# Kernel tuning notes

Measured on AMD Instinct MI355X. Metric: run time of the kernel, lower is better.

## Reference

```python
import jax, jax.numpy as jnp
import numpy as np

N, T, H, D = 384, 384, 768, 128  # turns, per-turn seq len, hidden, qk proj dim


def setup_inputs() -> dict:
    key = jax.random.key(0)
    kx, kwq, kwk, kbq, kbk = jax.random.split(key, 5)
    x = jax.random.normal(kx, (N, T, H), dtype=jnp.float32)
    Wq = jax.random.normal(kwq, (H, D), dtype=jnp.float32) / np.sqrt(H).astype(np.float32)
    bq = jax.random.normal(kbq, (D,), dtype=jnp.float32) * 0.02
    Wk = jax.random.normal(kwk, (H, D), dtype=jnp.float32) / np.sqrt(H).astype(np.float32)
    bk = jax.random.normal(kbk, (D,), dtype=jnp.float32) * 0.02
    return {"x": x, "Wq": Wq, "bq": bq, "Wk": Wk, "bk": bk}


def reference(x, Wq, bq, Wk, bk):
    # x: [N, T, H] -> q, k: [N, T, D]
    q = x @ Wq + bq
    k = x @ Wk + bk
    # Per-position dot products across turns: s[i, j, t] = <q[i,t], k[j,t]> / sqrt(D)
    s = jnp.einsum('itd,jtd->ijt', q, k) / jnp.sqrt(jnp.asarray(D, x.dtype))
    # Causal over turns: row i attends to turns j <= i. The original does a
    # JOINT softmax over all (j, t) pairs in rows 0..i (flattened), per i.
    causal = jnp.arange(N)[:, None] >= jnp.arange(N)[None, :]  # [N, N]
    s = jnp.where(causal[:, :, None], s, -jnp.inf)
    alpha = jax.nn.softmax(s.reshape(N, N * T), axis=-1).reshape(N, N, T)
    # new_x[i, t, :] = sum_j alpha[i, j, t] * x[j, t, :]
    out = jnp.einsum('ijt,jth->ith', alpha, x)
    # Row 0 is a pass-through in the original (the i == 0 branch).
    out = out.at[0].set(x[0])
    return out
```

## Files before the change

### kernel.cpp

```cpp
#include <hip/hip_runtime.h>
#include <hip/hip_bf16.h>
#include <math.h>

#define NT 384
#define TL 384
#define HD 768
#define DD 128
#define PT_T 86016

typedef __attribute__((ext_vector_type(8))) short bf16x8;
typedef __attribute__((ext_vector_type(8))) unsigned short u16x8;
typedef __attribute__((ext_vector_type(4))) float f32x4;

__device__ __forceinline__ unsigned short f2b(float f) {
    union { float f; unsigned int u; } v; v.f = f;
    unsigned int r = v.u + 0x7FFFu + ((v.u >> 16) & 1u);
    return (unsigned short)(r >> 16);
}

__global__ __launch_bounds__(256) void kw_prep(
    const float* __restrict__ Wq, const float* __restrict__ Wk,
    unsigned short* __restrict__ Wt)
{
    const int idx = blockIdx.x * 256 + threadIdx.x;
    const int k = idx >> 8, n = idx & 255;
    const float v = (n < DD) ? Wq[(size_t)k * DD + n] : Wk[(size_t)k * DD + (n - DD)];
    Wt[(size_t)n * HD + k] = f2b(v);
}

__global__ __launch_bounds__(256, 3) void k_proj(
    const float* __restrict__ x, const unsigned short* __restrict__ Wt,
    const float* __restrict__ bq, const float* __restrict__ bk,
    unsigned short* __restrict__ qg, unsigned short* __restrict__ kg)
{
    __shared__ unsigned short As[64 * 64];
    __shared__ unsigned short os2[64 * 264];
    const int tid = threadIdx.x;
    const int lane = tid & 63;
    const int w = tid >> 6;
    const int row0 = blockIdx.x * 64;
    const int n0w = w * 64;
    const int lr = lane & 15;
    const int lg = lane >> 4;

    f32x4 acc[4][4];
    #pragma unroll
    for (int m = 0; m < 4; ++m)
        #pragma unroll
        for (int n = 0; n < 4; ++n) acc[m][n] = (f32x4){0.f, 0.f, 0.f, 0.f};

    const int sm = tid >> 2;
    const int sc0 = (tid & 3) * 2;

    for (int k0 = 0; k0 < HD; k0 += 64) {
        __syncthreads();
        {
            const float* xp = x + (size_t)(row0 + sm) * HD + k0 + (tid & 3) * 16;
            u16x8 v0, v1;
            #pragma unroll
            for (int u4 = 0; u4 < 2; ++u4) {
                float4 f = *(const float4*)(xp + u4 * 4);
                v0[u4*4+0] = f2b(f.x); v0[u4*4+1] = f2b(f.y);
                v0[u4*4+2] = f2b(f.z); v0[u4*4+3] = f2b(f.w);
            }
            #pragma unroll
            for (int u4 = 0; u4 < 2; ++u4) {
                float4 f = *(const float4*)(xp + 8 + u4 * 4);
                v1[u4*4+0] = f2b(f.x); v1[u4*4+1] = f2b(f.y);
                v1[u4*4+2] = f2b(f.z); v1[u4*4+3] = f2b(f.w);
            }
            *(u16x8*)&As[sm * 64 + ((sc0     ^ (sm & 7)) * 8)] = v0;
            *(u16x8*)&As[sm * 64 + (((sc0+1) ^ (sm & 7)) * 8)] = v1;
        }
        __syncthreads();
        #pragma unroll
        for (int kk = 0; kk < 2; ++kk) {
            bf16x8 a[4], b[4];
            #pragma unroll
            for (int m = 0; m < 4; ++m) {
                const int mi = m * 16 + lr;
                const int phys = (lg + kk * 4) ^ (mi & 7);
                a[m] = *(const bf16x8*)&As[mi * 64 + phys * 8];
            }
            #pragma unroll
            for (int n = 0; n < 4; ++n) {
                const int ncol = n0w + n * 16 + lr;
                b[n] = *(const bf16x8*)(Wt + (size_t)ncol * HD + k0 + kk * 32 + lg * 8);
            }
            #pragma unroll
            for (int m = 0; m < 4; ++m)
                #pragma unroll
                for (int n = 0; n < 4; ++n)
                    acc[m][n] = __builtin_amdgcn_mfma_f32_16x16x32_bf16(a[m], b[n], acc[m][n], 0, 0, 0);
        }
    }
    const float scale = 0.08838834764831845f;
    const int ib = row0 / TL;
    const int tb = row0 % TL;
    __syncthreads();
    #pragma unroll
    for (int n = 0; n < 4; ++n) {
        const int ncol = n0w + n * 16 + lr;
        const bool isq = ncol < DD;
        const int d = isq ? ncol : ncol - DD;
        const float bias = isq ? bq[d] : bk[d];
        #pragma unroll
        for (int m = 0; m < 4; ++m)
            #pragma unroll
            for (int r = 0; r < 4; ++r) {
                const int trow = m * 16 + lg * 4 + r;
                float v = acc[m][n][r] + bias;
                if (isq) v *= scale;
                os2[trow * 264 + ncol] = f2b(v);
            }
    }
    __syncthreads();
    #pragma unroll
    for (int s = 0; s < 8; ++s) {
        const int flat = s * 256 + tid;
        const int arr  = flat >> 10;
        const int rem  = flat & 1023;
        const int trow = rem >> 4;
        const int c16  = rem & 15;
        unsigned short* dst = (arr ? kg : qg)
            + ((size_t)(tb + trow) * NT + ib) * DD + c16 * 8;
        *(u16x8*)dst = *(const u16x8*)&os2[trow * 264 + arr * 128 + c16 * 8];
    }
}

__global__ __launch_bounds__(256, 4) void k_xt(
    const float* __restrict__ x, unsigned short* __restrict__ xt)
{
    const int tid = threadIdx.x;
    const int hb = blockIdx.x % 3;
    const int jc = blockIdx.x / 3;
    const int t  = blockIdx.y;
    const int joblk   = tid & 3;
    const int h_local = tid >> 2;
    const int hbase = hb * 256 + h_local * 4;

    float4 v[8];
    #pragma unroll
    for (int r = 0; r < 8; ++r) {
        const int j = jc * 32 + joblk * 8 + r;
        v[r] = *(const float4*)&x[((size_t)j * TL + t) * HD + hbase];
    }
    #pragma unroll
    for (int e = 0; e < 4; ++e) {
        u16x8 w;
        w[0] = f2b(v[0][e]); w[1] = f2b(v[1][e]);
        w[2] = f2b(v[2][e]); w[3] = f2b(v[3][e]);
        w[4] = f2b(v[4][e]); w[5] = f2b(v[5][e]);
        w[6] = f2b(v[6][e]); w[7] = f2b(v[7][e]);
        *(u16x8*)&xt[(((size_t)t * 12 + jc) * HD + hbase + e) * 32 + joblk * 8] = w;
    }
}

__global__ __launch_bounds__(256, 4) void k_qk(
    const unsigned short* __restrict__ qg, const unsigned short* __restrict__ kg,
    unsigned short* __restrict__ Pt, float* __restrict__ lpart)
{
    __shared__ unsigned short pw[4096];
    __shared__ float red[4][64];
    const int tid = threadIdx.x, lane = tid & 63, w = tid >> 6;
    const int lr = lane & 15, lg = lane >> 4;
    const int bid = blockIdx.x;
    const int lid = (bid & 7) * (2304 / 8) + (bid >> 3);
    const int it = lid % 6, t = lid / 6;
    const int i0 = it * 64;
    unsigned short* ptile = Pt + (size_t)t * PT_T + 2048 * (size_t)(it * (it + 1));

    bf16x8 aq[4][4];
    #pragma unroll
    for (int m = 0; m < 4; ++m) {
        const unsigned short* qp = qg + ((size_t)t * NT + i0 + m * 16 + lr) * DD + lg * 8;
        #pragma unroll
        for (int kk = 0; kk < 4; ++kk) aq[m][kk] = *(const bf16x8*)(qp + kk * 32);
    }
    float psum[4][4];
    #pragma unroll
    for (int m = 0; m < 4; ++m)
        #pragma unroll
        for (int r = 0; r < 4; ++r) psum[m][r] = 0.f;

    for (int c = 0; c <= it; ++c) {
        const int j0 = c * 64;
        const unsigned short* kp = kg + ((size_t)t * NT + j0 + w * 16 + lr) * DD + lg * 8;
        bf16x8 bk8[4];
        #pragma unroll
        for (int kk = 0; kk < 4; ++kk) bk8[kk] = *(const bf16x8*)(kp + kk * 32);
        const int jg = j0 + w * 16 + lr;
        unsigned short* pws = pw + (w >> 1) * 2048 + (w & 1) * 16 + lr;
        #pragma unroll
        for (int m = 0; m < 4; ++m) {
            f32x4 s = (f32x4){0.f, 0.f, 0.f, 0.f};
            #pragma unroll
            for (int kk = 0; kk < 4; ++kk)
                s = __builtin_amdgcn_mfma_f32_16x16x32_bf16(aq[m][kk], bk8[kk], s, 0, 0, 0);
            #pragma unroll
            for (int r = 0; r < 4; ++r) {
                const int il = m * 16 + lg * 4 + r;
                const float wv = (jg <= i0 + il) ? __expf(s[r]) : 0.f;
                psum[m][r] += wv;
                pws[il * 32] = f2b(wv);
            }
        }
        __syncthreads();
        unsigned short* pdst = ptile + (size_t)c * 4096;
        #pragma unroll
        for (int s2 = 0; s2 < 2; ++s2) {
            const int flat = s2 * 256 + tid;
            *(u16x8*)&pdst[flat * 8] = *(const u16x8*)&pw[flat * 8];
        }
        __syncthreads();
    }
    #pragma unroll
    for (int off = 1; off < 16; off <<= 1)
        #pragma unroll
        for (int m = 0; m < 4; ++m)
            #pragma unroll
            for (int r = 0; r < 4; ++r)
                psum[m][r] += __shfl_xor(psum[m][r], off);
    if (lr == 0) {
        #pragma unroll
        for (int m = 0; m < 4; ++m)
            #pragma unroll
            for (int r = 0; r < 4; ++r)
                red[w][m * 16 + lg * 4 + r] = psum[m][r];
    }
    __syncthreads();
    if (tid < 64)
        lpart[(size_t)(i0 + tid) * TL + t] = red[0][tid] + red[1][tid] + red[2][tid] + red[3][tid];
}

__global__ __launch_bounds__(256) void k_lred(const float* __restrict__ lpart,
                                              float* __restrict__ linv)
{
    const int i = blockIdx.x;
    const int tid = threadIdx.x;
    float s = 0.f;
    for (int t = tid; t < TL; t += 256) s += lpart[(size_t)i * TL + t];
    #pragma unroll
    for (int off = 32; off >= 1; off >>= 1) s += __shfl_down(s, off);
    __shared__ float red[4];
    if ((tid & 63) == 0) red[tid >> 6] = s;
    __syncthreads();
    if (tid == 0) linv[i] = 1.f / (red[0] + red[1] + red[2] + red[3]);
}

__global__ __launch_bounds__(256, 3) void k_pv_g(
    const unsigned short* __restrict__ Pt, const unsigned short* __restrict__ xt,
    const float* __restrict__ linv, const float* __restrict__ x,
    float* __restrict__ out)
{
    __shared__ float os[32 * 260];
    const int tid = threadIdx.x, lane = tid & 63, w = tid >> 6;
    const int lr = lane & 15, lg = lane >> 4;
    const int bid = blockIdx.x;
    const int lid = (bid & 7) * (6912 / 8) + (bid >> 3);
    const int hb  = lid % 3;
    const int rem3 = lid / 3;
    const int it64 = rem3 % 6, t = rem3 / 6;
    const int i0 = it64 * 64;

    const unsigned short* pbase = Pt + (size_t)t * PT_T + 2048 * (size_t)(it64 * (it64 + 1))
                                + (size_t)lr * 32 + lg * 8;
    const unsigned short* xbase = xt + (((size_t)t * 12) * HD + hb * 256 + w * 64 + lr) * 32 + lg * 8;

    f32x4 acc[4][4];
    #pragma unroll
    for (int m = 0; m < 4; ++m)
        #pragma unroll
        for (int n = 0; n < 4; ++n) acc[m][n] = (f32x4){0.f, 0.f, 0.f, 0.f};

    bf16x8 paA0, paA1, paA2, paA3, bxA0, bxA1, bxA2, bxA3;
    bf16x8 paB0, paB1, paB2, paB3, bxB0, bxB1, bxB2, bxB3;

#define LOADSET(P0, P1, P2, P3, B0, B1, B2, B3, cc) do {                       \
        const unsigned short* pp_ = pbase + (size_t)(cc) * 2048;               \
        P0 = *(const bf16x8*)(pp_);                                            \
        P1 = *(const bf16x8*)(pp_ + 512);                                      \
        P2 = *(const bf16x8*)(pp_ + 1024);                                     \
        P3 = *(const bf16x8*)(pp_ + 1536);                                     \
        const unsigned short* xp_ = xbase + (size_t)(cc) * (HD * 32);          \
        B0 = *(const bf16x8*)(xp_);                                            \
        B1 = *(const bf16x8*)(xp_ + 512);                                      \
        B2 = *(const bf16x8*)(xp_ + 1024);                                     \
        B3 = *(const bf16x8*)(xp_ + 1536);                                     \
    } while (0)

#define MFMASET(P0, P1, P2, P3, B0, B1, B2, B3) do {                           \
        __builtin_amdgcn_s_setprio(1);                                         \
        acc[0][0] = __builtin_amdgcn_mfma_f32_16x16x32_bf16(P0, B0, acc[0][0], 0, 0, 0); \
        acc[1][0] = __builtin_amdgcn_mfma_f32_16x16x32_bf16(P1, B0, acc[1][0], 0, 0, 0); \
        acc[2][0] = __builtin_amdgcn_mfma_f32_16x16x32_bf16(P2, B0, acc[2][0], 0, 0, 0); \
        acc[3][0] = __builtin_amdgcn_mfma_f32_16x16x32_bf16(P3, B0, acc[3][0], 0, 0, 0); \
        acc[0][1] = __builtin_amdgcn_mfma_f32_16x16x32_bf16(P0, B1, acc[0][1], 0, 0, 0); \
        acc[1][1] = __builtin_amdgcn_mfma_f32_16x16x32_bf16(P1, B1, acc[1][1], 0, 0, 0); \
        acc[2][1] = __builtin_amdgcn_mfma_f32_16x16x32_bf16(P2, B1, acc[2][1], 0, 0, 0); \
        acc[3][1] = __builtin_amdgcn_mfma_f32_16x16x32_bf16(P3, B1, acc[3][1], 0, 0, 0); \
        acc[0][2] = __builtin_amdgcn_mfma_f32_16x16x32_bf16(P0, B2, acc[0][2], 0, 0, 0); \
        acc[1][2] = __builtin_amdgcn_mfma_f32_16x16x32_bf16(P1, B2, acc[1][2], 0, 0, 0); \
        acc[2][2] = __builtin_amdgcn_mfma_f32_16x16x32_bf16(P2, B2, acc[2][2], 0, 0, 0); \
        acc[3][2] = __builtin_amdgcn_mfma_f32_16x16x32_bf16(P3, B2, acc[3][2], 0, 0, 0); \
        acc[0][3] = __builtin_amdgcn_mfma_f32_16x16x32_bf16(P0, B3, acc[0][3], 0, 0, 0); \
        acc[1][3] = __builtin_amdgcn_mfma_f32_16x16x32_bf16(P1, B3, acc[1][3], 0, 0, 0); \
        acc[2][3] = __builtin_amdgcn_mfma_f32_16x16x32_bf16(P2, B3, acc[2][3], 0, 0, 0); \
        acc[3][3] = __builtin_amdgcn_mfma_f32_16x16x32_bf16(P3, B3, acc[3][3], 0, 0, 0); \
        __builtin_amdgcn_s_setprio(0);                                         \
    } while (0)

    const int nq = 2 * (it64 + 1);
    LOADSET(paA0, paA1, paA2, paA3, bxA0, bxA1, bxA2, bxA3, 0);
    for (int c = 0; c < nq; c += 2) {
        LOADSET(paB0, paB1, paB2, paB3, bxB0, bxB1, bxB2, bxB3, c + 1);
        MFMASET(paA0, paA1, paA2, paA3, bxA0, bxA1, bxA2, bxA3);
        if (c + 2 < nq)
            LOADSET(paA0, paA1, paA2, paA3, bxA0, bxA1, bxA2, bxA3, c + 2);
        MFMASET(paB0, paB1, paB2, paB3, bxB0, bxB1, bxB2, bxB3);
    }
#undef LOADSET
#undef MFMASET

    #pragma unroll
    for (int half = 0; half < 2; ++half) {
        if (half) __syncthreads();
        #pragma unroll
        for (int mm = 0; mm < 2; ++mm) {
            const int m = half * 2 + mm;
            #pragma unroll
            for (int r = 0; r < 4; ++r) {
                const int il = mm * 16 + lg * 4 + r;
                const float sc = linv[i0 + half * 32 + il];
                const int hl = w * 64 + lr;
                #pragma unroll
                for (int n = 0; n < 4; ++n)
                    os[il * 260 + hl + n * 16] = acc[m][n][r] * sc;
            }
        }
        __syncthreads();
        #pragma unroll
        for (int s2 = 0; s2 < 8; ++s2) {
            const int flat = s2 * 256 + tid;
            const int gi_l = flat >> 6, rm = flat & 63;
            const int gi = i0 + half * 32 + gi_l;
            float4 v;
            if (gi == 0) v = *(const float4*)&x[(size_t)t * HD + hb * 256 + rm * 4];
            else         v = *(const float4*)&os[gi_l * 260 + rm * 4];
            *(float4*)&out[((size_t)gi * TL + t) * HD + hb * 256 + rm * 4] = v;
        }
    }
}

__global__ __launch_bounds__(256, 4) void k_stats64(
    const unsigned short* __restrict__ qg, const unsigned short* __restrict__ kg,
    float* __restrict__ lpart)
{
    __shared__ float red[4][64];
    const int tid = threadIdx.x, lane = tid & 63, w = tid >> 6;
    const int lr = lane & 15, lg = lane >> 4;
    const int bid = blockIdx.x;
    const int lid = (bid & 7) * (2304 / 8) + (bid >> 3);
    const int it = lid % 6, t = lid / 6;
    const int i0 = it * 64;

    bf16x8 aq[4][4];
    #pragma unroll
    for (int m = 0; m < 4; ++m) {
        const unsigned short* qp = qg + ((size_t)t * NT + i0 + m * 16 + lr) * DD + lg * 8;
        #pragma unroll
        for (int kk = 0; kk < 4; ++kk) aq[m][kk] = *(const bf16x8*)(qp + kk * 32);
    }
    float psum[4][4];
    #pragma unroll
    for (int m = 0; m < 4; ++m)
        #pragma unroll
        for (int r = 0; r < 4; ++r) psum[m][r] = 0.f;

    for (int c = 0; c <= it; ++c) {
        const int j0 = c * 64;
        const unsigned short* kp = kg + ((size_t)t * NT + j0 + w * 16 + lr) * DD + lg * 8;
        bf16x8 bk8[4];
        #pragma unroll
        for (int kk = 0; kk < 4; ++kk) bk8[kk] = *(const bf16x8*)(kp + kk * 32);
        const int jg = j0 + w * 16 + lr;
        #pragma unroll
        for (int m = 0; m < 4; ++m) {
            f32x4 s = (f32x4){0.f, 0.f, 0.f, 0.f};
            #pragma unroll
            for (int kk = 0; kk < 4; ++kk)
                s = __builtin_amdgcn_mfma_f32_16x16x32_bf16(aq[m][kk], bk8[kk], s, 0, 0, 0);
            #pragma unroll
            for (int r = 0; r < 4; ++r) {
                const int ig = i0 + m * 16 + lg * 4 + r;
                psum[m][r] += (jg <= ig) ? __expf(s[r]) : 0.f;
            }
        }
    }
    #pragma unroll
    for (int off = 1; off < 16; off <<= 1)
        #pragma unroll
        for (int m = 0; m < 4; ++m)
            #pragma unroll
            for (int r = 0; r < 4; ++r)
                psum[m][r] += __shfl_xor(psum[m][r], off);
    if (lr == 0) {
        #pragma unroll
        for (int m = 0; m < 4; ++m)
            #pragma unroll
            for (int r = 0; r < 4; ++r)
                red[w][m * 16 + lg * 4 + r] = psum[m][r];
    }
    __syncthreads();
    if (tid < 64)
        lpart[(size_t)(i0 + tid) * TL + t] = red[0][tid] + red[1][tid] + red[2][tid] + red[3][tid];
}

__global__ __launch_bounds__(256, 4) void k_pv3(
    const unsigned short* __restrict__ qg, const unsigned short* __restrict__ kg,
    const unsigned short* __restrict__ xt, const float* __restrict__ linv,
    const float* __restrict__ x, float* __restrict__ out)
{
    __shared__ unsigned short P[32 * 64];
    const int tid = threadIdx.x, lane = tid & 63, w = tid >> 6;
    const int lr = lane & 15, lg = lane >> 4;
    const int bid = blockIdx.x;
    const int lid = (bid & 7) * (4608 / 8) + (bid >> 3);
    const int it = lid % 12, t = lid / 12;
    const int i0 = it * 32;
    const int h0 = blockIdx.y * 256 + w * 64;

    bf16x8 aq[2][4];
    #pragma unroll
    for (int m = 0; m < 2; ++m) {
        const unsigned short* qp = qg + ((size_t)t * NT + i0 + m * 16 + lr) * DD + lg * 8;
        #pragma unroll
        for (int kk = 0; kk < 4; ++kk) aq[m][kk] = *(const bf16x8*)(qp + kk * 32);
    }
    f32x4 acc[2][4];
    #pragma unroll
    for (int m = 0; m < 2; ++m)
        #pragma unroll
        for (int n = 0; n < 4; ++n) acc[m][n] = (f32x4){0.f, 0.f, 0.f, 0.f};

    const int nch = (i0 + 32 + 63) >> 6;
    for (int c = 0; c < nch; ++c) {
        const int j0 = c * 64;
        __syncthreads();
        f32x4 s[2] = { (f32x4){0,0,0,0}, (f32x4){0,0,0,0} };
        const unsigned short* kp = kg + ((size_t)t * NT + j0 + w * 16 + lr) * DD + lg * 8;
        #pragma unroll
        for (int kk = 0; kk < 4; ++kk) {
            const bf16x8 bk8 = *(const bf16x8*)(kp + kk * 32);
            s[0] = __builtin_amdgcn_mfma_f32_16x16x32_bf16(aq[0][kk], bk8, s[0], 0, 0, 0);
            s[1] = __builtin_amdgcn_mfma_f32_16x16x32_bf16(aq[1][kk], bk8, s[1], 0, 0, 0);
        }
        const int jg = j0 + w * 16 + lr;
        const int jl = w * 16 + lr;
        #pragma unroll
        for (int m = 0; m < 2; ++m)
            #pragma unroll
            for (int r = 0; r < 4; ++r) {
                const int il = m * 16 + lg * 4 + r;
                const float wv = (jg <= i0 + il) ? __expf(s[m][r]) : 0.f;
                P[il * 64 + (((jl >> 3) ^ (il & 7)) * 8) + (jl & 7)] = f2b(wv);
            }
        __syncthreads();
        #pragma unroll
        for (int kk2 = 0; kk2 < 2; ++kk2) {
            bf16x8 pa[2];
            #pragma unroll
            for (int m = 0; m < 2; ++m) {
                const int il = m * 16 + lr;
                const int ch = kk2 * 4 + lg;
                pa[m] = *(const bf16x8*)&P[il * 64 + ((ch ^ (il & 7)) * 8)];
            }
            const unsigned short* xp =
                xt + (((size_t)t * 12 + (j0 >> 5) + kk2) * HD + h0 + lr) * 32 + lg * 8;
            #pragma unroll
            for (int n = 0; n < 4; ++n) {
                const bf16x8 bx = *(const bf16x8*)(xp + n * 512);
                acc[0][n] = __builtin_amdgcn_mfma_f32_16x16x32_bf16(pa[0], bx, acc[0][n], 0, 0, 0);
                acc[1][n] = __builtin_amdgcn_mfma_f32_16x16x32_bf16(pa[1], bx, acc[1][n], 0, 0, 0);
            }
        }
    }
    #pragma unroll
    for (int m = 0; m < 2; ++m)
        #pragma unroll
        for (int r = 0; r < 4; ++r) {
            const int gi = i0 + m * 16 + lg * 4 + r;
            float* op = out + ((size_t)gi * TL + t) * HD + h0 + lr;
            if (gi == 0) {
                const float* xp0 = x + (size_t)t * HD + h0 + lr;
                #pragma unroll
                for (int n = 0; n < 4; ++n) op[n * 16] = xp0[n * 16];
            } else {
                const float sc = linv[gi];
                #pragma unroll
                for (int n = 0; n < 4; ++n) op[n * 16] = acc[m][n][r] * sc;
            }
        }
}

extern "C" void kernel_launch(void* const* d_in, const int* in_sizes, int n_in,
                              void* d_out, int out_size, void* d_ws, size_t ws_size,
                              hipStream_t stream)
{
    const float* x  = (const float*)d_in[0];
    const float* Wq = (const float*)d_in[1];
    const float* bq = (const float*)d_in[2];
    const float* Wk = (const float*)d_in[3];
    const float* bk = (const float*)d_in[4];
    float* out = (float*)d_out;

    unsigned short* Wt = (unsigned short*)d_ws;
    unsigned short* qb = Wt + (size_t)256 * HD;
    unsigned short* kb = qb + (size_t)NT * TL * DD;
    float* lpart = (float*)(kb + (size_t)NT * TL * DD);
    float* linv  = lpart + (size_t)NT * TL;
    unsigned short* xt = (unsigned short*)(linv + NT);
    unsigned short* Pt = xt + (size_t)TL * 12 * HD * 32;

    const size_t need = (size_t)((char*)(Pt + (size_t)TL * PT_T) - (char*)d_ws);
    const bool use_split = ws_size >= need;

    kw_prep<<<dim3(768), 256, 0, stream>>>(Wq, Wk, Wt);
    k_proj<<<dim3(NT * TL / 64), 256, 0, stream>>>(x, Wt, bq, bk, qb, kb);
    k_xt<<<dim3(36, TL), 256, 0, stream>>>(x, xt);
    if (use_split) {
        k_qk<<<dim3(2304), 256, 0, stream>>>(qb, kb, Pt, lpart);
        k_lred<<<dim3(NT), 256, 0, stream>>>(lpart, linv);
        k_pv_g<<<dim3(6912), 256, 0, stream>>>(Pt, xt, linv, x, out);
    } else {
        k_stats64<<<dim3(2304), 256, 0, stream>>>(qb, kb, lpart);
        k_lred<<<dim3(NT), 256, 0, stream>>>(lpart, linv);
        k_pv3<<<dim3(4608, 3), 256, 0, stream>>>(qb, kb, xt, linv, x, out);
    }
}
```

Before: 562.4 us.

## Fuse x transpose/bf16 conversion into projection kernel via shared-memory tile reuse

```diff
diff --git a/kernel.cpp b/kernel.cpp
--- a/kernel.cpp
+++ b/kernel.cpp
@@ -31,14 +31,17 @@
 __global__ __launch_bounds__(256, 3) void k_proj(
     const float* __restrict__ x, const unsigned short* __restrict__ Wt,
     const float* __restrict__ bq, const float* __restrict__ bk,
-    unsigned short* __restrict__ qg, unsigned short* __restrict__ kg)
+    unsigned short* __restrict__ qg, unsigned short* __restrict__ kg,
+    unsigned short* __restrict__ xt)
 {
     __shared__ unsigned short As[64 * 64];
     __shared__ unsigned short os2[64 * 264];
     const int tid = threadIdx.x;
     const int lane = tid & 63;
     const int w = tid >> 6;
-    const int row0 = blockIdx.x * 64;
+    const int it6 = blockIdx.x % 6;
+    const int t   = blockIdx.x / 6;
+    const int i0 = it6 * 64;
     const int n0w = w * 64;
     const int lr = lane & 15;
     const int lg = lane >> 4;
@@ -55,7 +58,7 @@
     for (int k0 = 0; k0 < HD; k0 += 64) {
         __syncthreads();
         {
-            const float* xp = x + (size_t)(row0 + sm) * HD + k0 + (tid & 3) * 16;
+            const float* xp = x + ((size_t)(i0 + sm) * TL + t) * HD + k0 + (tid & 3) * 16;
             u16x8 v0, v1;
             #pragma unroll
             for (int u4 = 0; u4 < 2; ++u4) {
@@ -93,10 +96,22 @@
                 for (int n = 0; n < 4; ++n)
                     acc[m][n] = __builtin_amdgcn_mfma_f32_16x16x32_bf16(a[m], b[n], acc[m][n], 0, 0, 0);
         }
+        #pragma unroll
+        for (int uu = 0; uu < 2; ++uu) {
+            const int u = uu * 256 + tid;
+            const int jc2   = u >> 8;
+            const int hl    = (u >> 2) & 63;
+            const int joblk = u & 3;
+            u16x8 wv;
+            #pragma unroll
+            for (int e = 0; e < 8; ++e) {
+                const int il = jc2 * 32 + joblk * 8 + e;
+                wv[e] = As[il * 64 + (((hl >> 3) ^ (il & 7)) * 8) + (hl & 7)];
+            }
+            *(u16x8*)&xt[(((size_t)t * 12 + (i0 >> 5) + jc2) * HD + k0 + hl) * 32 + joblk * 8] = wv;
+        }
     }
     const float scale = 0.08838834764831845f;
-    const int ib = row0 / TL;
-    const int tb = row0 % TL;
     __syncthreads();
     #pragma unroll
     for (int n = 0; n < 4; ++n) {
@@ -108,10 +123,10 @@
         for (int m = 0; m < 4; ++m)
             #pragma unroll
             for (int r = 0; r < 4; ++r) {
-                const int trow = m * 16 + lg * 4 + r;
+                const int il = m * 16 + lg * 4 + r;
                 float v = acc[m][n][r] + bias;
                 if (isq) v *= scale;
-                os2[trow * 264 + ncol] = f2b(v);
+                os2[il * 264 + ncol] = f2b(v);
             }
     }
     __syncthreads();
@@ -120,39 +135,11 @@
         const int flat = s * 256 + tid;
         const int arr  = flat >> 10;
         const int rem  = flat & 1023;
-        const int trow = rem >> 4;
+        const int irow = rem >> 4;
         const int c16  = rem & 15;
         unsigned short* dst = (arr ? kg : qg)
-            + ((size_t)(tb + trow) * NT + ib) * DD + c16 * 8;
-        *(u16x8*)dst = *(const u16x8*)&os2[trow * 264 + arr * 128 + c16 * 8];
-    }
-}
-
-__global__ __launch_bounds__(256, 4) void k_xt(
-    const float* __restrict__ x, unsigned short* __restrict__ xt)
-{
-    const int tid = threadIdx.x;
-    const int hb = blockIdx.x % 3;
-    const int jc = blockIdx.x / 3;
-    const int t  = blockIdx.y;
-    const int joblk   = tid & 3;
-    const int h_local = tid >> 2;
-    const int hbase = hb * 256 + h_local * 4;
-
-    float4 v[8];
-    #pragma unroll
-    for (int r = 0; r < 8; ++r) {
-        const int j = jc * 32 + joblk * 8 + r;
-        v[r] = *(const float4*)&x[((size_t)j * TL + t) * HD + hbase];
-    }
-    #pragma unroll
-    for (int e = 0; e < 4; ++e) {
-        u16x8 w;
-        w[0] = f2b(v[0][e]); w[1] = f2b(v[1][e]);
-        w[2] = f2b(v[2][e]); w[3] = f2b(v[3][e]);
-        w[4] = f2b(v[4][e]); w[5] = f2b(v[5][e]);
-        w[6] = f2b(v[6][e]); w[7] = f2b(v[7][e]);
-        *(u16x8*)&xt[(((size_t)t * 12 + jc) * HD + hbase + e) * 32 + joblk * 8] = w;
+            + ((size_t)t * NT + i0 + irow) * DD + c16 * 8;
+        *(u16x8*)dst = *(const u16x8*)&os2[irow * 264 + arr * 128 + c16 * 8];
     }
 }
 
@@ -526,8 +513,7 @@
     const bool use_split = ws_size >= need;
 
     kw_prep<<<dim3(768), 256, 0, stream>>>(Wq, Wk, Wt);
-    k_proj<<<dim3(NT * TL / 64), 256, 0, stream>>>(x, Wt, bq, bk, qb, kb);
-    k_xt<<<dim3(36, TL), 256, 0, stream>>>(x, xt);
+    k_proj<<<dim3(NT * TL / 64), 256, 0, stream>>>(x, Wt, bq, bk, qb, kb, xt);
     if (use_split) {
         k_qk<<<dim3(2304), 256, 0, stream>>>(qb, kb, Pt, lpart);
         k_lred<<<dim3(NT), 256, 0, stream>>>(lpart, linv);
```

Result: faster. 473.0 us, median of 2 (-15.9%).
